# Performance work log

Hardware: AMD Instinct MI355X
Metric: run time of the kernel (lower is better)

## Reference

```python
import jax, jax.numpy as jnp
from jax import lax
import numpy as np

B = 16
C1, H1, W1 = 512, 28, 28   # wide_resnet50_2 layer2 @ 224px
C2, H2, W2 = 1024, 14, 14  # wide_resnet50_2 layer3 @ 224px
M = 15000                  # memory bank max size (embedding_max_len)
D = C1 + C2                # 1536
IMG = 224                  # input_size
NUM_NEIGHBORS = 9
SIGMA = 4.0                # anomalib AnomalyMapGenerator default
KS = 2 * int(4.0 * SIGMA + 0.5) + 1  # 33 (kornia kernel-size rule)


def setup_inputs() -> dict:
    key = jax.random.key(0)
    k1, k2, k3 = jax.random.split(key, 3)
    return {
        "feat1": jax.random.normal(k1, (B, C1, H1, W1), dtype=jnp.float32),
        "feat2": jax.random.normal(k2, (B, C2, H2, W2), dtype=jnp.float32),
        "memory_bank": jax.random.normal(k3, (M, D), dtype=jnp.float32),
    }


def _avg_pool3(x):
    # torch.nn.AvgPool2d(3, 1, 1) with count_include_pad=True -> sum window / 9
    s = lax.reduce_window(x, 0.0, lax.add, (1, 1, 3, 3), (1, 1, 1, 1),
                          [(0, 0), (0, 0), (1, 1), (1, 1)])
    return s / 9.0


def _edist(x, y):
    x_norm = jnp.sum(x * x, axis=-1, keepdims=True)
    y_norm = jnp.sum(y * y, axis=-1, keepdims=True)
    res = x_norm - 2.0 * jnp.matmul(x, jnp.swapaxes(y, -2, -1)) + jnp.swapaxes(y_norm, -2, -1)
    return jnp.sqrt(jnp.maximum(res, 0.0))


def _gauss_kernel():
    t = jnp.arange(KS, dtype=jnp.float32) - (KS - 1) / 2.0
    g = jnp.exp(-(t * t) / (2.0 * SIGMA * SIGMA))
    return g / jnp.sum(g)


def _gaussian_blur(x):
    # separable depthwise gaussian blur with reflect padding (kornia GaussianBlur2d)
    g = _gauss_kernel()
    p = KS // 2
    x = jnp.pad(x, ((0, 0), (0, 0), (p, p), (p, p)), mode='reflect')
    dn = ('NCHW', 'OIHW', 'NCHW')
    x = lax.conv_general_dilated(x, g.reshape(1, 1, KS, 1), (1, 1), 'VALID', dimension_numbers=dn)
    x = lax.conv_general_dilated(x, g.reshape(1, 1, 1, KS), (1, 1), 'VALID', dimension_numbers=dn)
    return x


def reference(feat1, feat2, memory_bank):
    # 1. feature pooling + hierarchical embedding concat
    f1 = _avg_pool3(feat1)                                   # [B,512,28,28]
    f2 = _avg_pool3(feat2)                                   # [B,1024,14,14]
    f2 = jax.image.resize(f2, (f2.shape[0], f2.shape[1], H1, W1), 'bilinear')
    emb = jnp.concatenate([f1, f2], axis=1)                  # [B,1536,28,28]
    b, d = emb.shape[0], emb.shape[1]
    e = emb.transpose(0, 2, 3, 1).reshape(-1, d)             # [B*P, D]

    # 2. brute-force 1-NN against memory bank
    dist = _edist(e, memory_bank)                            # [N, M]
    patch_scores = jnp.min(dist, axis=1)                     # [N]
    locations = jnp.argmin(dist, axis=1)                     # [N]
    P = H1 * W1
    ps = patch_scores.reshape(b, P)
    loc = locations.reshape(b, P)

    # 3. image-level anomaly score with num_neighbors=9 re-weighting
    bidx = jnp.arange(b)
    mp = jnp.argmax(ps, axis=1)                              # [B]
    max_feat = e.reshape(b, P, d)[bidx, mp]                  # [B,D]
    score = ps[bidx, mp]                                     # [B]
    nn_index = loc[bidx, mp]                                 # [B]
    nn_sample = memory_bank[nn_index]                        # [B,D]
    d_nb = _edist(nn_sample, memory_bank)                    # [B,M]
    _, support = lax.top_k(-d_nb, NUM_NEIGHBORS)             # [B,9] smallest
    sup_feats = memory_bank[support]                         # [B,9,D]
    d2 = _edist(max_feat[:, None, :], sup_feats)             # [B,1,9]
    weights = (1.0 - jax.nn.softmax(d2[:, 0, :], axis=1))[:, 0]
    pred_score = weights * score                             # [B]

    # 4. anomaly map: upsample patch scores to input size + gaussian blur
    amap = ps.reshape(b, 1, H1, W1)
    amap = jax.image.resize(amap, (b, 1, IMG, IMG), 'bilinear')
    amap = _gaussian_blur(amap)                              # [B,1,224,224]
    return amap, pred_score
```

## Files before the change

### kernel.cpp

```cpp
#include <hip/hip_runtime.h>
#include <stdint.h>

#define B_    16
#define C1_   512
#define C2_   1024
#define H2_   14
#define D_    1536
#define P_    784
#define N_    12544
#define M_    15000
#define MPAD_ 15104
#define MT1_  118
#define MT2_  59
#define NT_   98
#define IMG_  224
#define KS_   33

typedef unsigned short u16;
typedef unsigned int   u32;
typedef unsigned long long u64;

__device__ __forceinline__ u16 f2bf(float x) {
    u32 u = __float_as_uint(x);
    u = u + 0x7fffu + ((u >> 16) & 1u);
    return (u16)(u >> 16);
}
__device__ __forceinline__ float bf2f(u16 h) {
    return __uint_as_float(((u32)h) << 16);
}
__device__ __forceinline__ u32 ordf(float f) {
    u32 u = __float_as_uint(f);
    return (u & 0x80000000u) ? ~u : (u | 0x80000000u);
}
__device__ __forceinline__ float unordf(u32 o) {
    u32 u = (o & 0x80000000u) ? (o ^ 0x80000000u) : ~o;
    return __uint_as_float(u);
}

__global__ void k_pool2(const float* __restrict__ feat2, float* __restrict__ pooled2) {
    int idx = blockIdx.x * 256 + threadIdx.x;
    if (idx >= B_ * C2_ * H2_ * H2_) return;
    int x = idx % 14, y = (idx / 14) % 14, bc = idx / 196;
    const float* src = feat2 + (size_t)bc * 196;
    float s = 0.f;
    for (int dy = -1; dy <= 1; ++dy) {
        int yy = y + dy; if (yy < 0 || yy > 13) continue;
        for (int dx = -1; dx <= 1; ++dx) {
            int xx = x + dx; if (xx < 0 || xx > 13) continue;
            s += src[yy * 14 + xx];
        }
    }
    pooled2[idx] = s * (1.f / 9.f);
}

__global__ __launch_bounds__(192)
void k_bank(const float* __restrict__ bank, u16* __restrict__ Bh,
            u16* __restrict__ Bl, float* __restrict__ ynorm) {
    int m = blockIdx.x, tid = threadIdx.x;
    float nrm = 0.f;
    float v[8];
    if (m < M_) {
        const float4* src = (const float4*)(bank + (size_t)m * D_ + tid * 8);
        float4 a = src[0], b = src[1];
        v[0]=a.x; v[1]=a.y; v[2]=a.z; v[3]=a.w; v[4]=b.x; v[5]=b.y; v[6]=b.z; v[7]=b.w;
#pragma unroll
        for (int i = 0; i < 8; ++i) nrm += v[i] * v[i];
    } else {
#pragma unroll
        for (int i = 0; i < 8; ++i) v[i] = 0.f;
    }
    u32 hw[4], lw[4];
#pragma unroll
    for (int i = 0; i < 4; ++i) {
        u16 h0 = f2bf(v[2*i]),   l0 = f2bf(v[2*i]   - bf2f(h0));
        u16 h1 = f2bf(v[2*i+1]), l1 = f2bf(v[2*i+1] - bf2f(h1));
        hw[i] = (u32)h0 | ((u32)h1 << 16);
        lw[i] = (u32)l0 | ((u32)l1 << 16);
    }
    *(uint4*)(Bh + (size_t)m * D_ + tid * 8) = make_uint4(hw[0], hw[1], hw[2], hw[3]);
    *(uint4*)(Bl + (size_t)m * D_ + tid * 8) = make_uint4(lw[0], lw[1], lw[2], lw[3]);
    __shared__ float red[3];
    for (int off = 32; off; off >>= 1) nrm += __shfl_down(nrm, off, 64);
    int wave = tid >> 6, lane = tid & 63;
    if (lane == 0) red[wave] = nrm;
    __syncthreads();
    if (tid == 0) {
        float t = red[0] + red[1] + red[2];
        ynorm[m] = (m < M_) ? t : __uint_as_float(0x7f800000u);
    }
}

__global__ __launch_bounds__(256)
void k_embed(const float* __restrict__ feat1, const float* __restrict__ pooled2,
             u16* __restrict__ Ah, u16* __restrict__ Al, float* __restrict__ xnorm) {
    __shared__ float sF[3 * 64 * 29];
    __shared__ float xn[28];
    const int tid = threadIdx.x, lane = tid & 63, wave = tid >> 6;
    const int b = blockIdx.x / 28, y = blockIdx.x % 28;
    const int brow = b * P_ + y * 28;
    if (tid < 28) xn[tid] = 0.f;

    float sy = y * 0.5f - 0.25f;
    int iy = (int)floorf(sy);
    float fy = sy - iy;
    int y0 = min(max(iy, 0), 13), y1 = min(max(iy + 1, 0), 13);
    __syncthreads();

    for (int cc = 0; cc < 8; ++cc) {
        for (int j = tid; j < 3 * 64 * 28; j += 256) {
            int x = j % 28, c = (j / 28) % 64, r = j / (28 * 64);
            int yy = y - 1 + r;
            float v = 0.f;
            if (yy >= 0 && yy < 28)
                v = feat1[((size_t)(b * C1_ + cc * 64 + c)) * 784 + yy * 28 + x];
            sF[(r * 64 + c) * 29 + x] = v;
        }
        __syncthreads();
        for (int it = 0; it < 7; ++it) {
            int x = it * 4 + wave, c = lane;
            float s = 0.f;
#pragma unroll
            for (int r = 0; r < 3; ++r) {
                int base = (r * 64 + c) * 29;
                if (x > 0) s += sF[base + x - 1];
                s += sF[base + x];
                if (x < 27) s += sF[base + x + 1];
            }
            float v = s * (1.f / 9.f);
            int col = cc * 64 + c;
            size_t off = (size_t)(brow + x) * D_ + col;
            u16 h = f2bf(v);
            Ah[off] = h; Al[off] = f2bf(v - bf2f(h));
            float vv = v * v;
            for (int m = 1; m < 64; m <<= 1) vv += __shfl_xor(vv, m, 64);
            if (lane == 0) atomicAdd(&xn[x], vv);
        }
        __syncthreads();
    }

    for (int cc = 0; cc < 16; ++cc) {
        for (int it = 0; it < 7; ++it) {
            int x = it * 4 + wave, c = lane;
            const float* sp = pooled2 + ((size_t)(b * C2_ + cc * 64 + c)) * 196;
            float sx = x * 0.5f - 0.25f;
            int ix = (int)floorf(sx);
            float fx = sx - ix;
            int x0 = min(max(ix, 0), 13), x1 = min(max(ix + 1, 0), 13);
            float v = (1.f - fy) * ((1.f - fx) * sp[y0 * 14 + x0] + fx * sp[y0 * 14 + x1])
                    + fy * ((1.f - fx) * sp[y1 * 14 + x0] + fx * sp[y1 * 14 + x1]);
            int col = C1_ + cc * 64 + c;
            size_t off = (size_t)(brow + x) * D_ + col;
            u16 h = f2bf(v);
            Ah[off] = h; Al[off] = f2bf(v - bf2f(h));
            float vv = v * v;
            for (int m = 1; m < 64; m <<= 1) vv += __shfl_xor(vv, m, 64);
            if (lane == 0) atomicAdd(&xn[x], vv);
        }
    }
    __syncthreads();
    if (tid < 28) xnorm[brow + tid] = xn[tid];
}

typedef __bf16 bf16x8 __attribute__((ext_vector_type(8)));
typedef float  f32x16 __attribute__((ext_vector_type(16)));

#define GLD16(dst, src) __builtin_amdgcn_global_load_lds( \
    (const __attribute__((address_space(1))) void*)(src), \
    (__attribute__((address_space(3))) void*)(dst), 16, 0, 0)

__global__ __launch_bounds__(256, 2)
void k_gemm1(const u16* __restrict__ Ah, const u16* __restrict__ Bh,
             const float* __restrict__ ynorm, float* __restrict__ partf) {
    __shared__ u16 sA[2][128 * 32];
    __shared__ u16 sB[2][256 * 32];
    __shared__ float smin[128][2];

    const int tid = threadIdx.x, lane = tid & 63, wave = tid >> 6;
    const int GM = 4, nig = GM * NT_;
    const int grp = blockIdx.x / nig, rem = blockIdx.x - grp * nig;
    const int first = grp * GM;
    const int gsz = (MT2_ - first) < GM ? (MT2_ - first) : GM;
    const int mt = first + rem % gsz;
    const int pt = rem / gsz;
    const int p0 = pt * 128, m0 = mt * 256;

    f32x16 acc[2][4];
#pragma unroll
    for (int i = 0; i < 2; ++i)
#pragma unroll
        for (int j = 0; j < 4; ++j)
#pragma unroll
            for (int e = 0; e < 16; ++e) acc[i][j][e] = 0.f;

    const int srow = lane >> 2;
    const int schunk8 = ((lane & 3) ^ ((lane >> 3) & 3)) * 8;
    const int wr = (wave >> 1) * 64, wc = (wave & 1) * 128;
    const int rA = lane & 31, kh = lane >> 5;
    const int rsw = (lane >> 1) & 3;

    const int arow0 = (wave * 2 + 0) * 16 + srow, arow1 = (wave * 2 + 1) * 16 + srow;
    const u16* gA0 = Ah + (size_t)(p0 + arow0) * D_ + schunk8;
    const u16* gA1 = Ah + (size_t)(p0 + arow1) * D_ + schunk8;
    const u16* gB0 = Bh + (size_t)(m0 + (wave * 4 + 0) * 16 + srow) * D_ + schunk8;
    const u16* gB1 = Bh + (size_t)(m0 + (wave * 4 + 1) * 16 + srow) * D_ + schunk8;
    const u16* gB2 = Bh + (size_t)(m0 + (wave * 4 + 2) * 16 + srow) * D_ + schunk8;
    const u16* gB3 = Bh + (size_t)(m0 + (wave * 4 + 3) * 16 + srow) * D_ + schunk8;
    u16* lA0 = &sA[0][(wave * 2 + 0) * 512]; u16* lA1 = &sA[0][(wave * 2 + 1) * 512];
    u16* lB0 = &sB[0][(wave * 4 + 0) * 512]; u16* lB1 = &sB[0][(wave * 4 + 1) * 512];
    u16* lB2 = &sB[0][(wave * 4 + 2) * 512]; u16* lB3 = &sB[0][(wave * 4 + 3) * 512];
    const size_t bufA = 128 * 32, bufB = 256 * 32;

    GLD16(lA0, gA0); GLD16(lA1, gA1);
    GLD16(lB0, gB0); GLD16(lB1, gB1); GLD16(lB2, gB2); GLD16(lB3, gB3);

    for (int kt = 0; kt < 48; ++kt) {
        const int cur = kt & 1, nxt = cur ^ 1;
        __syncthreads();
        if (kt < 47) {
            const int k1 = (kt + 1) * 32;
            GLD16(lA0 + nxt * bufA, gA0 + k1); GLD16(lA1 + nxt * bufA, gA1 + k1);
            GLD16(lB0 + nxt * bufB, gB0 + k1); GLD16(lB1 + nxt * bufB, gB1 + k1);
            GLD16(lB2 + nxt * bufB, gB2 + k1); GLD16(lB3 + nxt * bufB, gB3 + k1);
        }
        bf16x8 af[2][2], bfr[2][4];
#pragma unroll
        for (int ks = 0; ks < 2; ++ks) {
            const int slot = ((ks * 2 + kh) ^ rsw) * 8;
#pragma unroll
            for (int ti = 0; ti < 2; ++ti)
                af[ks][ti] = *(const bf16x8*)&sA[cur][(wr + ti * 32 + rA) * 32 + slot];
#pragma unroll
            for (int tj = 0; tj < 4; ++tj)
                bfr[ks][tj] = *(const bf16x8*)&sB[cur][(wc + tj * 32 + rA) * 32 + slot];
        }
#pragma unroll
        for (int ks = 0; ks < 2; ++ks)
#pragma unroll
            for (int ti = 0; ti < 2; ++ti)
#pragma unroll
                for (int tj = 0; tj < 4; ++tj)
                    acc[ti][tj] = __builtin_amdgcn_mfma_f32_32x32x16_bf16(
                        af[ks][ti], bfr[ks][tj], acc[ti][tj], 0, 0, 0);
    }

    const int c32 = lane & 31;
    float yn[4];
#pragma unroll
    for (int tj = 0; tj < 4; ++tj) yn[tj] = ynorm[m0 + wc + tj * 32 + c32];
#pragma unroll
    for (int ti = 0; ti < 2; ++ti) {
#pragma unroll
        for (int reg = 0; reg < 16; ++reg) {
            const int rloc = wr + ti * 32 + (reg & 3) + 8 * (reg >> 2) + 4 * kh;
            float v = __uint_as_float(0x7f800000u);
#pragma unroll
            for (int tj = 0; tj < 4; ++tj)
                v = fminf(v, yn[tj] - 2.0f * acc[ti][tj][reg]);
#pragma unroll
            for (int msk = 1; msk < 32; msk <<= 1)
                v = fminf(v, __shfl_xor(v, msk, 64));
            if (c32 == 0) smin[rloc][wave & 1] = v;
        }
    }
    __syncthreads();
    if (tid < 128)
        partf[(size_t)mt * N_ + p0 + tid] = fminf(smin[tid][0], smin[tid][1]);
}

__global__ void k_reduce(const float* __restrict__ partf, const float* __restrict__ xnorm,
                         float* __restrict__ ps) {
    int n = blockIdx.x * 128 + threadIdx.x;
    float best = __uint_as_float(0x7f800000u);
    for (int t = 0; t < MT2_; ++t)
        best = fminf(best, partf[(size_t)t * N_ + n]);
    ps[n] = sqrtf(fmaxf(best + xnorm[n], 0.f));
}

__global__ void k_cand(const float* __restrict__ ps, int* __restrict__ candrow) {
    int b = blockIdx.x, tid = threadIdx.x;
    __shared__ u64 red[4];
    u64 prev = ~0ull;
    for (int j = 0; j < 8; ++j) {
        u64 best = 0;
        for (int p = tid; p < P_; p += 256) {
            u64 pk = ((u64)ordf(ps[b * P_ + p]) << 32) | (u32)(~(u32)p);
            if (pk < prev && pk > best) best = pk;
        }
        for (int msk = 1; msk < 64; msk <<= 1) {
            u64 o = __shfl_xor(best, msk, 64);
            best = o > best ? o : best;
        }
        int wave = tid >> 6, lane = tid & 63;
        if (lane == 0) red[wave] = best;
        __syncthreads();
        u64 m = red[0];
        for (int w = 1; w < 4; ++w) m = red[w] > m ? red[w] : m;
        if (tid == 0) candrow[b * 8 + j] = b * P_ + (int)(~(u32)m);
        prev = m;
        __syncthreads();
    }
}

__global__ __launch_bounds__(256)
void k_gexact(const u16* __restrict__ Ah, const u16* __restrict__ Al,
              const u16* __restrict__ Bh, const u16* __restrict__ Bl,
              const int* __restrict__ candrow, float* __restrict__ pdot) {
    __shared__ u16 sA[2][128 * 32];
    __shared__ u16 sB[2][128 * 32];
    __shared__ int scand[128];

    const int tid = threadIdx.x;
    const int lane = tid & 63, wave = tid >> 6;
    const int mt = blockIdx.x, slice = blockIdx.y;
    const int m0 = mt * 128;
    if (tid < 128) scand[tid] = candrow[tid];

    f32x16 acc[2][2];
#pragma unroll
    for (int i = 0; i < 2; ++i)
#pragma unroll
        for (int j = 0; j < 2; ++j)
#pragma unroll
            for (int e = 0; e < 16; ++e) acc[i][j][e] = 0.f;

    const int srow = lane >> 2;
    const int scol = ((lane & 3) ^ ((lane >> 3) & 3)) * 8;
    const int wr = (wave >> 1) * 64, wc = (wave & 1) * 64;
    const int rA = lane & 31;
    const int sw = (lane >> 1) & 3;
    __syncthreads();

    for (int kt = slice * 12; kt < slice * 12 + 12; ++kt) {
        const int k0 = kt * 32;
#pragma unroll
        for (int s = 0; s < 2; ++s) {
            const int slab = wave * 2 + s;
            const int row = slab * 16 + srow;
            const int grow = scand[row];
            GLD16(&sA[0][slab * 512], Ah + (size_t)grow * D_ + k0 + scol);
            GLD16(&sA[1][slab * 512], Al + (size_t)grow * D_ + k0 + scol);
            GLD16(&sB[0][slab * 512], Bh + (size_t)(m0 + row) * D_ + k0 + scol);
            GLD16(&sB[1][slab * 512], Bl + (size_t)(m0 + row) * D_ + k0 + scol);
        }
        __syncthreads();
#pragma unroll
        for (int ks = 0; ks < 2; ++ks) {
            const int co = ((ks * 2 + (lane >> 5)) ^ sw) * 8;
            bf16x8 ah0 = *(const bf16x8*)&sA[0][(wr + rA) * 32 + co];
            bf16x8 ah1 = *(const bf16x8*)&sA[0][(wr + 32 + rA) * 32 + co];
            bf16x8 al0 = *(const bf16x8*)&sA[1][(wr + rA) * 32 + co];
            bf16x8 al1 = *(const bf16x8*)&sA[1][(wr + 32 + rA) * 32 + co];
            bf16x8 bh0 = *(const bf16x8*)&sB[0][(wc + rA) * 32 + co];
            bf16x8 bh1 = *(const bf16x8*)&sB[0][(wc + 32 + rA) * 32 + co];
            bf16x8 bl0 = *(const bf16x8*)&sB[1][(wc + rA) * 32 + co];
            bf16x8 bl1 = *(const bf16x8*)&sB[1][(wc + 32 + rA) * 32 + co];
            acc[0][0] = __builtin_amdgcn_mfma_f32_32x32x16_bf16(ah0, bh0, acc[0][0], 0, 0, 0);
            acc[0][1] = __builtin_amdgcn_mfma_f32_32x32x16_bf16(ah0, bh1, acc[0][1], 0, 0, 0);
            acc[1][0] = __builtin_amdgcn_mfma_f32_32x32x16_bf16(ah1, bh0, acc[1][0], 0, 0, 0);
            acc[1][1] = __builtin_amdgcn_mfma_f32_32x32x16_bf16(ah1, bh1, acc[1][1], 0, 0, 0);
            acc[0][0] = __builtin_amdgcn_mfma_f32_32x32x16_bf16(ah0, bl0, acc[0][0], 0, 0, 0);
            acc[0][1] = __builtin_amdgcn_mfma_f32_32x32x16_bf16(ah0, bl1, acc[0][1], 0, 0, 0);
            acc[1][0] = __builtin_amdgcn_mfma_f32_32x32x16_bf16(ah1, bl0, acc[1][0], 0, 0, 0);
            acc[1][1] = __builtin_amdgcn_mfma_f32_32x32x16_bf16(ah1, bl1, acc[1][1], 0, 0, 0);
            acc[0][0] = __builtin_amdgcn_mfma_f32_32x32x16_bf16(al0, bh0, acc[0][0], 0, 0, 0);
            acc[0][1] = __builtin_amdgcn_mfma_f32_32x32x16_bf16(al0, bh1, acc[0][1], 0, 0, 0);
            acc[1][0] = __builtin_amdgcn_mfma_f32_32x32x16_bf16(al1, bh0, acc[1][0], 0, 0, 0);
            acc[1][1] = __builtin_amdgcn_mfma_f32_32x32x16_bf16(al1, bh1, acc[1][1], 0, 0, 0);
        }
        __syncthreads();
    }

    const int wrB = wave >> 1, wcB = wave & 1;
    const int half = lane >> 5, c32 = lane & 31;
    float* base = pdot + ((size_t)(slice * MT1_ + mt) * 128) * 128;
#pragma unroll
    for (int ti = 0; ti < 2; ++ti) {
#pragma unroll
        for (int reg = 0; reg < 16; ++reg) {
            const int rloc = wrB * 64 + ti * 32 + 4 * half + (reg & 3) + 8 * (reg >> 2);
#pragma unroll
            for (int tj = 0; tj < 2; ++tj)
                base[(size_t)rloc * 128 + wcB * 64 + tj * 32 + c32] = acc[ti][tj][reg];
        }
    }
}

__global__ void k_pickc(const float* __restrict__ pdot, const float* __restrict__ ynorm,
                        u64* __restrict__ candmin) {
    int i = blockIdx.x, tid = threadIdx.x;
    __shared__ u64 red[4];
    u64 best = ~0ull;
    for (int m = tid; m < MPAD_; m += 256) {
        float dot = 0.f;
#pragma unroll
        for (int s = 0; s < 4; ++s)
            dot += pdot[((size_t)(s * MT1_ + (m >> 7)) * 128 + i) * 128 + (m & 127)];
        float v = ynorm[m] - 2.f * dot;
        u64 pk = ((u64)ordf(v) << 32) | (u32)m;
        best = pk < best ? pk : best;
    }
    for (int msk = 1; msk < 64; msk <<= 1) {
        u64 o = __shfl_xor(best, msk, 64);
        best = o < best ? o : best;
    }
    int wave = tid >> 6, lane = tid & 63;
    if (lane == 0) red[wave] = best;
    __syncthreads();
    if (tid == 0) {
        u64 m = red[0];
        for (int w = 1; w < 4; ++w) m = red[w] < m ? red[w] : m;
        candmin[i] = m;
    }
}

__global__ void k_pick(const u64* __restrict__ candmin, const float* __restrict__ xnorm,
                       const int* __restrict__ candrow, int* __restrict__ mprow,
                       int* __restrict__ nnidx, float* __restrict__ score) {
    __shared__ float sps[128];
    __shared__ int sloc[128];
    int i = threadIdx.x;
    u64 best = candmin[i];
    float val = unordf((u32)(best >> 32)) + xnorm[candrow[i]];
    sps[i] = sqrtf(fmaxf(val, 0.f));
    sloc[i] = (int)(u32)best;
    __syncthreads();
    if (i < B_) {
        float bs = -1.f; int bj = 0; int brw = 1 << 30;
        for (int j = 0; j < 8; ++j) {
            int idx = i * 8 + j;
            float v = sps[idx];
            int row = candrow[idx];
            if (v > bs || (v == bs && row < brw)) { bs = v; bj = idx; brw = row; }
        }
        mprow[i] = brw;
        nnidx[i] = sloc[bj];
        score[i] = bs;
    }
}

__global__ void k_dnb(const float* __restrict__ bank, const float* __restrict__ ynorm,
                      const int* __restrict__ nnidx, float* __restrict__ dnb) {
    int wave = threadIdx.x >> 6, lane = threadIdx.x & 63;
    int m = blockIdx.x * 4 + wave;
    if (m >= M_) return;
    const float4* br = (const float4*)(bank + (size_t)m * D_);
    float acc[B_];
#pragma unroll
    for (int b = 0; b < B_; ++b) acc[b] = 0.f;
#pragma unroll
    for (int p = 0; p < 6; ++p) {
        float4 c = br[p * 64 + lane];
#pragma unroll
        for (int b = 0; b < B_; ++b) {
            const float4* nr = (const float4*)(bank + (size_t)nnidx[b] * D_);
            float4 a = nr[p * 64 + lane];
            acc[b] += a.x * c.x + a.y * c.y + a.z * c.z + a.w * c.w;
        }
    }
    float ym = ynorm[m];
    float keep = 0.f;
#pragma unroll
    for (int b = 0; b < B_; ++b) {
        float v = acc[b];
        for (int msk = 1; msk < 64; msk <<= 1) v += __shfl_xor(v, msk, 64);
        if (lane == b) keep = v;
    }
    if (lane < B_) {
        float ynn = ynorm[nnidx[lane]];
        dnb[lane * M_ + m] = sqrtf(fmaxf(ynn - 2.f * keep + ym, 0.f));
    }
}

__global__ void k_top9a(const float* __restrict__ dnb, u64* __restrict__ cand9) {
    int blk = blockIdx.x;
    int b = blk >> 3, ch = blk & 7;
    int base = ch * 1875;
    int tid = threadIdx.x;
    __shared__ u64 red[4];
    u64 prev = 0;
    for (int p = 0; p < 9; ++p) {
        u64 best = ~0ull;
        for (int i = tid; i < 1875; i += 256) {
            float v = dnb[b * M_ + base + i];
            u64 pk = ((u64)ordf(v) << 32) | (u32)(base + i);
            if (pk > prev && pk < best) best = pk;
        }
        for (int msk = 1; msk < 64; msk <<= 1) {
            u64 o = __shfl_xor(best, msk, 64);
            best = o < best ? o : best;
        }
        int wave = tid >> 6, lane = tid & 63;
        if (lane == 0) red[wave] = best;
        __syncthreads();
        u64 m = red[0];
        for (int w = 1; w < 4; ++w) m = red[w] < m ? red[w] : m;
        if (tid == 0) cand9[blk * 9 + p] = m;
        prev = m;
        __syncthreads();
    }
}
__global__ void k_top9b(const u64* __restrict__ cand9, int* __restrict__ support) {
    int b = blockIdx.x, lane = threadIdx.x;
    u64 v0 = lane < 72 ? cand9[b * 72 + lane] : ~0ull;
    u64 v1 = (lane + 64) < 72 ? cand9[b * 72 + lane + 64] : ~0ull;
    u64 prev = 0;
    for (int p = 0; p < 9; ++p) {
        u64 best = ~0ull;
        if (v0 > prev && v0 < best) best = v0;
        if (v1 > prev && v1 < best) best = v1;
        for (int msk = 1; msk < 64; msk <<= 1) {
            u64 o = __shfl_xor(best, msk, 64);
            best = o < best ? o : best;
        }
        if (lane == 0) support[b * 9 + p] = (int)(u32)best;
        prev = best;
    }
}

__global__ void k_final(const u16* __restrict__ Ah, const u16* __restrict__ Al,
                        const float* __restrict__ bank, const float* __restrict__ ynorm,
                        const float* __restrict__ xnorm, const int* __restrict__ mprow,
                        const int* __restrict__ support, const float* __restrict__ score,
                        float* __restrict__ out_score) {
    int b = blockIdx.x;
    int wave = threadIdx.x >> 6, lane = threadIdx.x & 63;
    __shared__ float d2s[9];
    int row = mprow[b];
    float xn = xnorm[row];
    for (int s = wave; s < 9; s += 4) {
        int sup = support[b * 9 + s];
        float acc = 0.f;
        for (int p = 0; p < 24; ++p) {
            int k = p * 64 + lane;
            float e = bf2f(Ah[(size_t)row * D_ + k]) + bf2f(Al[(size_t)row * D_ + k]);
            acc += e * bank[(size_t)sup * D_ + k];
        }
        for (int msk = 1; msk < 64; msk <<= 1) acc += __shfl_xor(acc, msk, 64);
        if (lane == 0) d2s[s] = sqrtf(fmaxf(xn - 2.f * acc + ynorm[sup], 0.f));
    }
    __syncthreads();
    if (threadIdx.x == 0) {
        float mx = d2s[0];
        for (int i = 1; i < 9; ++i) mx = fmaxf(mx, d2s[i]);
        float den = 0.f;
        for (int i = 0; i < 9; ++i) den += expf(d2s[i] - mx);
        float w = 1.f - expf(d2s[0] - mx) / den;
        out_score[b] = w * score[b];
    }
}

__global__ void k_upsample(const float* __restrict__ ps, float* __restrict__ U) {
    int idx = blockIdx.x * 256 + threadIdx.x;
    if (idx >= B_ * IMG_ * IMG_) return;
    int x = idx % IMG_, y = (idx / IMG_) % IMG_, b = idx / (IMG_ * IMG_);
    float sx = x * 0.125f - 0.4375f, sy = y * 0.125f - 0.4375f;
    int ix = (int)floorf(sx), iy = (int)floorf(sy);
    float fx = sx - ix, fy = sy - iy;
    int x0 = min(max(ix, 0), 27), x1 = min(max(ix + 1, 0), 27);
    int y0 = min(max(iy, 0), 27), y1 = min(max(iy + 1, 0), 27);
    const float* p = ps + b * P_;
    U[idx] = (1.f - fy) * ((1.f - fx) * p[y0 * 28 + x0] + fx * p[y0 * 28 + x1])
           + fy * ((1.f - fx) * p[y1 * 28 + x0] + fx * p[y1 * 28 + x1]);
}

__global__ void k_blurh(const float* __restrict__ U, float* __restrict__ T) {
    __shared__ float g[KS_];
    __shared__ float gs;
    int tid = threadIdx.x;
    if (tid < KS_) { float d = tid - 16.f; g[tid] = expf(-(d * d) / 32.0f); }
    __syncthreads();
    if (tid == 0) { float s = 0.f; for (int i = 0; i < KS_; ++i) s += g[i]; gs = 1.f / s; }
    __syncthreads();
    int idx = blockIdx.x * 256 + tid;
    if (idx >= B_ * IMG_ * IMG_) return;
    int x = idx % IMG_, rowbase = idx - x;
    float a = 0.f;
    for (int t = 0; t < KS_; ++t) {
        int xx = x + t - 16;
        xx = xx < 0 ? -xx : (xx > 223 ? 446 - xx : xx);
        a += g[t] * U[rowbase + xx];
    }
    T[idx] = a * gs;
}
__global__ void k_blurv(const float* __restrict__ T, float* __restrict__ out) {
    __shared__ float g[KS_];
    __shared__ float gs;
    int tid = threadIdx.x;
    if (tid < KS_) { float d = tid - 16.f; g[tid] = expf(-(d * d) / 32.0f); }
    __syncthreads();
    if (tid == 0) { float s = 0.f; for (int i = 0; i < KS_; ++i) s += g[i]; gs = 1.f / s; }
    __syncthreads();
    int idx = blockIdx.x * 256 + tid;
    if (idx >= B_ * IMG_ * IMG_) return;
    int x = idx % IMG_, y = (idx / IMG_) % IMG_, b = idx / (IMG_ * IMG_);
    float a = 0.f;
    for (int t = 0; t < KS_; ++t) {
        int yy = y + t - 16;
        yy = yy < 0 ? -yy : (yy > 223 ? 446 - yy : yy);
        a += g[t] * T[(b * IMG_ + yy) * IMG_ + x];
    }
    out[idx] = a * gs;
}

extern "C" void kernel_launch(void* const* d_in, const int* in_sizes, int n_in,
                              void* d_out, int out_size, void* d_ws, size_t ws_size,
                              hipStream_t stream) {
    const float* feat1 = (const float*)d_in[0];
    const float* feat2 = (const float*)d_in[1];
    const float* bank  = (const float*)d_in[2];
    float* out = (float*)d_out;
    char* ws = (char*)d_ws;

    size_t o = 0;
    u16* Ah = (u16*)(ws + o); o += (size_t)N_ * D_ * 2;
    u16* Al = (u16*)(ws + o); o += (size_t)N_ * D_ * 2;
    size_t o_Bh = o;
    u16* Bh = (u16*)(ws + o); o += (size_t)MPAD_ * D_ * 2;
    u16* Bl = (u16*)(ws + o); o += (size_t)MPAD_ * D_ * 2;
    size_t o_scr = o;
    float* pooled2 = (float*)(ws + o_scr);
    float* partf   = (float*)(ws + o_scr);
    size_t r1 = (size_t)MT2_ * N_ * 4, r2 = (size_t)B_ * C2_ * 196 * 4;
    o += (r1 > r2 ? r1 : r2);
    float* xnorm = (float*)(ws + o); o += (size_t)N_ * 4;
    float* ynorm = (float*)(ws + o); o += (size_t)MPAD_ * 4;
    float* ps    = (float*)(ws + o); o += (size_t)N_ * 4;
    int* candrow = (int*)(ws + o);   o += 512;
    float* pdot  = (float*)(ws + o); o += (size_t)4 * MT1_ * 128 * 128 * 4;
    u64* candmin = (u64*)(ws + o);   o += 128 * 8;
    float* dnb   = (float*)(ws + o); o += (size_t)B_ * M_ * 4;
    u64* cand9   = (u64*)(ws + o);   o += 128 * 9 * 8;
    int*   mprow = (int*)(ws + o);   o += 64;
    int*   nnidx = (int*)(ws + o);   o += 64;
    float* score = (float*)(ws + o); o += 64;
    int* support = (int*)(ws + o);   o += 9 * B_ * 4;
    float* U = (float*)(ws + o_Bh);
    float* T = (float*)(ws + o_Bh + (size_t)B_ * IMG_ * IMG_ * 4);

    k_pool2<<<(B_ * C2_ * H2_ * H2_ + 255) / 256, 256, 0, stream>>>(feat2, pooled2);
    k_bank<<<MPAD_, 192, 0, stream>>>(bank, Bh, Bl, ynorm);
    k_embed<<<B_ * 28, 256, 0, stream>>>(feat1, pooled2, Ah, Al, xnorm);
    k_gemm1<<<MT2_ * NT_, 256, 0, stream>>>(Ah, Bh, ynorm, partf);
    k_reduce<<<NT_, 128, 0, stream>>>(partf, xnorm, ps);
    k_cand<<<B_, 256, 0, stream>>>(ps, candrow);
    k_gexact<<<dim3(MT1_, 4), 256, 0, stream>>>(Ah, Al, Bh, Bl, candrow, pdot);
    k_pickc<<<128, 256, 0, stream>>>(pdot, ynorm, candmin);
    k_pick<<<1, 128, 0, stream>>>(candmin, xnorm, candrow, mprow, nnidx, score);
    k_dnb<<<(M_ + 3) / 4, 256, 0, stream>>>(bank, ynorm, nnidx, dnb);
    k_top9a<<<128, 256, 0, stream>>>(dnb, cand9);
    k_top9b<<<B_, 64, 0, stream>>>(cand9, support);
    k_final<<<B_, 256, 0, stream>>>(Ah, Al, bank, ynorm, xnorm, mprow, support, score,
                                    out + (size_t)B_ * IMG_ * IMG_);
    k_upsample<<<(B_ * IMG_ * IMG_ + 255) / 256, 256, 0, stream>>>(ps, U);
    k_blurh<<<(B_ * IMG_ * IMG_ + 255) / 256, 256, 0, stream>>>(U, T);
    k_blurv<<<(B_ * IMG_ * IMG_ + 255) / 256, 256, 0, stream>>>(T, out);
}
```

Before: 1.322 ms.

## Pre-pack GEMM operands into MFMA fragment layout and load directly from global

The embedding and memory-bank conversion kernels now write bf16 operands in a packed layout that matches the MFMA 32x32x16 fragment order. This lets k_gemm1 and the B side of k_gexact read fragments straight from global memory and drop the LDS staging, double buffering and barriers. The aim is to remove LDS traffic and sync overhead in the main distance GEMM. In exchange, operand reuse across waves now depends on L1/L2 caches instead of explicit shared-memory tiling, k_embed does extra scattered 2-byte stores, and the workspace aliasing is rearranged.

```diff
diff --git a/kernel.cpp b/kernel.cpp
--- a/kernel.cpp
+++ b/kernel.cpp
@@ -6,6 +6,7 @@
 #define C2_   1024
 #define H2_   14
 #define D_    1536
+#define K16_  96
 #define P_    784
 #define N_    12544
 #define M_    15000
@@ -36,6 +37,7 @@
     u32 u = (o & 0x80000000u) ? (o ^ 0x80000000u) : ~o;
     return __uint_as_float(u);
 }
+
 
 __global__ void k_pool2(const float* __restrict__ feat2, float* __restrict__ pooled2) {
     int idx = blockIdx.x * 256 + threadIdx.x;
@@ -54,8 +56,8 @@
 }
 
 __global__ __launch_bounds__(192)
-void k_bank(const float* __restrict__ bank, u16* __restrict__ Bh,
-            u16* __restrict__ Bl, float* __restrict__ ynorm) {
+void k_bank(const float* __restrict__ bank, u16* __restrict__ Bph,
+            u16* __restrict__ Bpl, float* __restrict__ ynorm) {
     int m = blockIdx.x, tid = threadIdx.x;
     float nrm = 0.f;
     float v[8];
@@ -77,10 +79,14 @@
         hw[i] = (u32)h0 | ((u32)h1 << 16);
         lw[i] = (u32)l0 | ((u32)l1 << 16);
     }
-    *(uint4*)(Bh + (size_t)m * D_ + tid * 8) = make_uint4(hw[0], hw[1], hw[2], hw[3]);
-    *(uint4*)(Bl + (size_t)m * D_ + tid * 8) = make_uint4(lw[0], lw[1], lw[2], lw[3]);
+    int c = tid * 8;
+    int k16 = c >> 4, kh = (c >> 3) & 1;
+    int mt2 = m >> 8, r = m & 255, gb = r >> 5, rA = r & 31;
+    size_t off = ((((size_t)mt2 * K16_ + k16) * 8 + gb) * 64 + kh * 32 + rA) * 8;
+    *(uint4*)(Bph + off) = make_uint4(hw[0], hw[1], hw[2], hw[3]);
+    *(uint4*)(Bpl + off) = make_uint4(lw[0], lw[1], lw[2], lw[3]);
     __shared__ float red[3];
-    for (int off = 32; off; off >>= 1) nrm += __shfl_down(nrm, off, 64);
+    for (int offr = 32; offr; offr >>= 1) nrm += __shfl_down(nrm, offr, 64);
     int wave = tid >> 6, lane = tid & 63;
     if (lane == 0) red[wave] = nrm;
     __syncthreads();
@@ -90,9 +96,20 @@
     }
 }
 
+__device__ __forceinline__ void emb_store(u16* Ah, u16* Al, u16* Aph,
+                                          int n, int col, float v) {
+    u16 h = f2bf(v);
+    size_t off = (size_t)n * D_ + col;
+    Ah[off] = h; Al[off] = f2bf(v - bf2f(h));
+    int pt = n >> 7, r = n & 127, g = r >> 5, rA = r & 31;
+    int k16 = col >> 4, kh = (col >> 3) & 1, j = col & 7;
+    Aph[((((size_t)pt * K16_ + k16) * 4 + g) * 64 + kh * 32 + rA) * 8 + j] = h;
+}
+
 __global__ __launch_bounds__(256)
 void k_embed(const float* __restrict__ feat1, const float* __restrict__ pooled2,
-             u16* __restrict__ Ah, u16* __restrict__ Al, float* __restrict__ xnorm) {
+             u16* __restrict__ Ah, u16* __restrict__ Al, u16* __restrict__ Aph,
+             float* __restrict__ xnorm) {
     __shared__ float sF[3 * 64 * 29];
     __shared__ float xn[28];
     const int tid = threadIdx.x, lane = tid & 63, wave = tid >> 6;
@@ -127,10 +144,7 @@
                 if (x < 27) s += sF[base + x + 1];
             }
             float v = s * (1.f / 9.f);
-            int col = cc * 64 + c;
-            size_t off = (size_t)(brow + x) * D_ + col;
-            u16 h = f2bf(v);
-            Ah[off] = h; Al[off] = f2bf(v - bf2f(h));
+            emb_store(Ah, Al, Aph, brow + x, cc * 64 + c, v);
             float vv = v * v;
             for (int m = 1; m < 64; m <<= 1) vv += __shfl_xor(vv, m, 64);
             if (lane == 0) atomicAdd(&xn[x], vv);
@@ -148,10 +162,7 @@
             int x0 = min(max(ix, 0), 13), x1 = min(max(ix + 1, 0), 13);
             float v = (1.f - fy) * ((1.f - fx) * sp[y0 * 14 + x0] + fx * sp[y0 * 14 + x1])
                     + fy * ((1.f - fx) * sp[y1 * 14 + x0] + fx * sp[y1 * 14 + x1]);
-            int col = C1_ + cc * 64 + c;
-            size_t off = (size_t)(brow + x) * D_ + col;
-            u16 h = f2bf(v);
-            Ah[off] = h; Al[off] = f2bf(v - bf2f(h));
+            emb_store(Ah, Al, Aph, brow + x, C1_ + cc * 64 + c, v);
             float vv = v * v;
             for (int m = 1; m < 64; m <<= 1) vv += __shfl_xor(vv, m, 64);
             if (lane == 0) atomicAdd(&xn[x], vv);
@@ -164,17 +175,10 @@
 typedef __bf16 bf16x8 __attribute__((ext_vector_type(8)));
 typedef float  f32x16 __attribute__((ext_vector_type(16)));
 
-#define GLD16(dst, src) __builtin_amdgcn_global_load_lds( \
-    (const __attribute__((address_space(1))) void*)(src), \
-    (__attribute__((address_space(3))) void*)(dst), 16, 0, 0)
-
 __global__ __launch_bounds__(256, 2)
-void k_gemm1(const u16* __restrict__ Ah, const u16* __restrict__ Bh,
+void k_gemm1(const u16* __restrict__ Aph, const u16* __restrict__ Bph,
              const float* __restrict__ ynorm, float* __restrict__ partf) {
-    __shared__ u16 sA[2][128 * 32];
-    __shared__ u16 sB[2][256 * 32];
     __shared__ float smin[128][2];
-
     const int tid = threadIdx.x, lane = tid & 63, wave = tid >> 6;
     const int GM = 4, nig = GM * NT_;
     const int grp = blockIdx.x / nig, rem = blockIdx.x - grp * nig;
@@ -192,58 +196,30 @@
 #pragma unroll
             for (int e = 0; e < 16; ++e) acc[i][j][e] = 0.f;
 
-    const int srow = lane >> 2;
-    const int schunk8 = ((lane & 3) ^ ((lane >> 3) & 3)) * 8;
     const int wr = (wave >> 1) * 64, wc = (wave & 1) * 128;
-    const int rA = lane & 31, kh = lane >> 5;
-    const int rsw = (lane >> 1) & 3;
-
-    const int arow0 = (wave * 2 + 0) * 16 + srow, arow1 = (wave * 2 + 1) * 16 + srow;
-    const u16* gA0 = Ah + (size_t)(p0 + arow0) * D_ + schunk8;
-    const u16* gA1 = Ah + (size_t)(p0 + arow1) * D_ + schunk8;
-    const u16* gB0 = Bh + (size_t)(m0 + (wave * 4 + 0) * 16 + srow) * D_ + schunk8;
-    const u16* gB1 = Bh + (size_t)(m0 + (wave * 4 + 1) * 16 + srow) * D_ + schunk8;
-    const u16* gB2 = Bh + (size_t)(m0 + (wave * 4 + 2) * 16 + srow) * D_ + schunk8;
-    const u16* gB3 = Bh + (size_t)(m0 + (wave * 4 + 3) * 16 + srow) * D_ + schunk8;
-    u16* lA0 = &sA[0][(wave * 2 + 0) * 512]; u16* lA1 = &sA[0][(wave * 2 + 1) * 512];
-    u16* lB0 = &sB[0][(wave * 4 + 0) * 512]; u16* lB1 = &sB[0][(wave * 4 + 1) * 512];
-    u16* lB2 = &sB[0][(wave * 4 + 2) * 512]; u16* lB3 = &sB[0][(wave * 4 + 3) * 512];
-    const size_t bufA = 128 * 32, bufB = 256 * 32;
-
-    GLD16(lA0, gA0); GLD16(lA1, gA1);
-    GLD16(lB0, gB0); GLD16(lB1, gB1); GLD16(lB2, gB2); GLD16(lB3, gB3);
-
-    for (int kt = 0; kt < 48; ++kt) {
-        const int cur = kt & 1, nxt = cur ^ 1;
-        __syncthreads();
-        if (kt < 47) {
-            const int k1 = (kt + 1) * 32;
-            GLD16(lA0 + nxt * bufA, gA0 + k1); GLD16(lA1 + nxt * bufA, gA1 + k1);
-            GLD16(lB0 + nxt * bufB, gB0 + k1); GLD16(lB1 + nxt * bufB, gB1 + k1);
-            GLD16(lB2 + nxt * bufB, gB2 + k1); GLD16(lB3 + nxt * bufB, gB3 + k1);
-        }
-        bf16x8 af[2][2], bfr[2][4];
-#pragma unroll
-        for (int ks = 0; ks < 2; ++ks) {
-            const int slot = ((ks * 2 + kh) ^ rsw) * 8;
-#pragma unroll
-            for (int ti = 0; ti < 2; ++ti)
-                af[ks][ti] = *(const bf16x8*)&sA[cur][(wr + ti * 32 + rA) * 32 + slot];
+    const u16* aB = Aph + ((size_t)pt * K16_ * 4 + (wr >> 5)) * 512 + lane * 8;
+    const u16* bB = Bph + ((size_t)mt * K16_ * 8 + (wc >> 5)) * 512 + lane * 8;
+
+#pragma unroll 4
+    for (int k16 = 0; k16 < K16_; ++k16) {
+        bf16x8 af[2], bfr[4];
+        const u16* ak = aB + (size_t)k16 * 4 * 512;
+        const u16* bk = bB + (size_t)k16 * 8 * 512;
+        af[0]  = *(const bf16x8*)(ak);
+        af[1]  = *(const bf16x8*)(ak + 512);
+        bfr[0] = *(const bf16x8*)(bk);
+        bfr[1] = *(const bf16x8*)(bk + 512);
+        bfr[2] = *(const bf16x8*)(bk + 1024);
+        bfr[3] = *(const bf16x8*)(bk + 1536);
+#pragma unroll
+        for (int ti = 0; ti < 2; ++ti)
 #pragma unroll
             for (int tj = 0; tj < 4; ++tj)
-                bfr[ks][tj] = *(const bf16x8*)&sB[cur][(wc + tj * 32 + rA) * 32 + slot];
-        }
-#pragma unroll
-        for (int ks = 0; ks < 2; ++ks)
-#pragma unroll
-            for (int ti = 0; ti < 2; ++ti)
-#pragma unroll
-                for (int tj = 0; tj < 4; ++tj)
-                    acc[ti][tj] = __builtin_amdgcn_mfma_f32_32x32x16_bf16(
-                        af[ks][ti], bfr[ks][tj], acc[ti][tj], 0, 0, 0);
-    }
-
-    const int c32 = lane & 31;
+                acc[ti][tj] = __builtin_amdgcn_mfma_f32_32x32x16_bf16(
+                    af[ti], bfr[tj], acc[ti][tj], 0, 0, 0);
+    }
+
+    const int c32 = lane & 31, kh = lane >> 5;
     float yn[4];
 #pragma unroll
     for (int tj = 0; tj < 4; ++tj) yn[tj] = ynorm[m0 + wc + tj * 32 + c32];
@@ -301,18 +277,20 @@
     }
 }
 
+#define GLD16(dst, src) __builtin_amdgcn_global_load_lds( \
+    (const __attribute__((address_space(1))) void*)(src), \
+    (__attribute__((address_space(3))) void*)(dst), 16, 0, 0)
+
 __global__ __launch_bounds__(256)
 void k_gexact(const u16* __restrict__ Ah, const u16* __restrict__ Al,
-              const u16* __restrict__ Bh, const u16* __restrict__ Bl,
+              const u16* __restrict__ Bph, const u16* __restrict__ Bpl,
               const int* __restrict__ candrow, float* __restrict__ pdot) {
     __shared__ u16 sA[2][128 * 32];
-    __shared__ u16 sB[2][128 * 32];
     __shared__ int scand[128];
 
     const int tid = threadIdx.x;
     const int lane = tid & 63, wave = tid >> 6;
     const int mt = blockIdx.x, slice = blockIdx.y;
-    const int m0 = mt * 128;
     if (tid < 128) scand[tid] = candrow[tid];
 
     f32x16 acc[2][2];
@@ -328,6 +306,7 @@
     const int wr = (wave >> 1) * 64, wc = (wave & 1) * 64;
     const int rA = lane & 31;
     const int sw = (lane >> 1) & 3;
+    const size_t bbase = (((size_t)(mt >> 1) * K16_) * 8 + (mt & 1) * 4 + (wc >> 5)) * 512 + lane * 8;
     __syncthreads();
 
     for (int kt = slice * 12; kt < slice * 12 + 12; ++kt) {
@@ -339,21 +318,20 @@
             const int grow = scand[row];
             GLD16(&sA[0][slab * 512], Ah + (size_t)grow * D_ + k0 + scol);
             GLD16(&sA[1][slab * 512], Al + (size_t)grow * D_ + k0 + scol);
-            GLD16(&sB[0][slab * 512], Bh + (size_t)(m0 + row) * D_ + k0 + scol);
-            GLD16(&sB[1][slab * 512], Bl + (size_t)(m0 + row) * D_ + k0 + scol);
         }
         __syncthreads();
 #pragma unroll
         for (int ks = 0; ks < 2; ++ks) {
             const int co = ((ks * 2 + (lane >> 5)) ^ sw) * 8;
+            const size_t bo = bbase + (size_t)(kt * 2 + ks) * 8 * 512;
             bf16x8 ah0 = *(const bf16x8*)&sA[0][(wr + rA) * 32 + co];
             bf16x8 ah1 = *(const bf16x8*)&sA[0][(wr + 32 + rA) * 32 + co];
             bf16x8 al0 = *(const bf16x8*)&sA[1][(wr + rA) * 32 + co];
             bf16x8 al1 = *(const bf16x8*)&sA[1][(wr + 32 + rA) * 32 + co];
-            bf16x8 bh0 = *(const bf16x8*)&sB[0][(wc + rA) * 32 + co];
-            bf16x8 bh1 = *(const bf16x8*)&sB[0][(wc + 32 + rA) * 32 + co];
-            bf16x8 bl0 = *(const bf16x8*)&sB[1][(wc + rA) * 32 + co];
-            bf16x8 bl1 = *(const bf16x8*)&sB[1][(wc + 32 + rA) * 32 + co];
+            bf16x8 bh0 = *(const bf16x8*)(Bph + bo);
+            bf16x8 bh1 = *(const bf16x8*)(Bph + bo + 512);
+            bf16x8 bl0 = *(const bf16x8*)(Bpl + bo);
+            bf16x8 bl1 = *(const bf16x8*)(Bpl + bo + 512);
             acc[0][0] = __builtin_amdgcn_mfma_f32_32x32x16_bf16(ah0, bh0, acc[0][0], 0, 0, 0);
             acc[0][1] = __builtin_amdgcn_mfma_f32_32x32x16_bf16(ah0, bh1, acc[0][1], 0, 0, 0);
             acc[1][0] = __builtin_amdgcn_mfma_f32_32x32x16_bf16(ah1, bh0, acc[1][0], 0, 0, 0);
@@ -611,12 +589,17 @@
     float* out = (float*)d_out;
     char* ws = (char*)d_ws;
 
+    const size_t apack_sz = (size_t)NT_ * K16_ * 4 * 512 * 2;
+    const size_t bpack_sz = (size_t)MT2_ * K16_ * 8 * 512 * 2;
+
     size_t o = 0;
-    u16* Ah = (u16*)(ws + o); o += (size_t)N_ * D_ * 2;
-    u16* Al = (u16*)(ws + o); o += (size_t)N_ * D_ * 2;
-    size_t o_Bh = o;
-    u16* Bh = (u16*)(ws + o); o += (size_t)MPAD_ * D_ * 2;
-    u16* Bl = (u16*)(ws + o); o += (size_t)MPAD_ * D_ * 2;
+    u16* Ah  = (u16*)(ws + o); o += (size_t)N_ * D_ * 2;
+    u16* Al  = (u16*)(ws + o); o += (size_t)N_ * D_ * 2;
+    size_t o_Ap = o;
+    u16* Aph = (u16*)(ws + o); o += apack_sz;
+    size_t o_Bp = o;
+    u16* Bph = (u16*)(ws + o); o += bpack_sz;
+    u16* Bpl = (u16*)(ws + o); o += bpack_sz;
     size_t o_scr = o;
     float* pooled2 = (float*)(ws + o_scr);
     float* partf   = (float*)(ws + o_scr);
@@ -626,7 +609,6 @@
     float* ynorm = (float*)(ws + o); o += (size_t)MPAD_ * 4;
     float* ps    = (float*)(ws + o); o += (size_t)N_ * 4;
     int* candrow = (int*)(ws + o);   o += 512;
-    float* pdot  = (float*)(ws + o); o += (size_t)4 * MT1_ * 128 * 128 * 4;
     u64* candmin = (u64*)(ws + o);   o += 128 * 8;
     float* dnb   = (float*)(ws + o); o += (size_t)B_ * M_ * 4;
     u64* cand9   = (u64*)(ws + o);   o += 128 * 9 * 8;
@@ -634,16 +616,17 @@
     int*   nnidx = (int*)(ws + o);   o += 64;
     float* score = (float*)(ws + o); o += 64;
     int* support = (int*)(ws + o);   o += 9 * B_ * 4;
-    float* U = (float*)(ws + o_Bh);
-    float* T = (float*)(ws + o_Bh + (size_t)B_ * IMG_ * IMG_ * 4);
+    float* pdot  = (float*)(ws + o_Ap);
+    float* U = (float*)(ws + o_Bp);
+    float* T = (float*)(ws + o_Bp + (size_t)B_ * IMG_ * IMG_ * 4);
 
     k_pool2<<<(B_ * C2_ * H2_ * H2_ + 255) / 256, 256, 0, stream>>>(feat2, pooled2);
-    k_bank<<<MPAD_, 192, 0, stream>>>(bank, Bh, Bl, ynorm);
-    k_embed<<<B_ * 28, 256, 0, stream>>>(feat1, pooled2, Ah, Al, xnorm);
-    k_gemm1<<<MT2_ * NT_, 256, 0, stream>>>(Ah, Bh, ynorm, partf);
+    k_bank<<<MPAD_, 192, 0, stream>>>(bank, Bph, Bpl, ynorm);
+    k_embed<<<B_ * 28, 256, 0, stream>>>(feat1, pooled2, Ah, Al, Aph, xnorm);
+    k_gemm1<<<MT2_ * NT_, 256, 0, stream>>>(Aph, Bph, ynorm, partf);
     k_reduce<<<NT_, 128, 0, stream>>>(partf, xnorm, ps);
     k_cand<<<B_, 256, 0, stream>>>(ps, candrow);
-    k_gexact<<<dim3(MT1_, 4), 256, 0, stream>>>(Ah, Al, Bh, Bl, candrow, pdot);
+    k_gexact<<<dim3(MT1_, 4), 256, 0, stream>>>(Ah, Al, Bph, Bpl, candrow, pdot);
     k_pickc<<<128, 256, 0, stream>>>(pdot, ynorm, candmin);
     k_pick<<<1, 128, 0, stream>>>(candmin, xnorm, candrow, mprow, nnidx, score);
     k_dnb<<<(M_ + 3) / 4, 256, 0, stream>>>(bank, ynorm, nnidx, dnb);
```

Result: faster. 1.253 ms (-5.2%).
